# Optimization experiments

Hardware: AMD Instinct MI355X
Metric: run time of the kernel (lower is better)

Reference implementation:

```python
import jax, jax.numpy as jnp
import numpy as np

N_NODES = 100000   # num_nodes
N_EDGES = 50000    # num_hyperedges
M = 1600000        # num incidences
D = 64             # hidden_size
N_LAYERS = 1


def setup_inputs() -> dict:
    key = jax.random.key(0)
    k1, k2, k3 = jax.random.split(key, 3)
    x = jax.random.normal(k1, (N_NODES, D), dtype=jnp.float32)
    node_idx = jax.random.randint(k2, (M,), 0, N_NODES, dtype=jnp.int32)
    edge_idx = jax.random.randint(k3, (M,), 0, N_EDGES, dtype=jnp.int32)
    edge_weight = jnp.ones((N_EDGES,), dtype=jnp.float32)
    return {"x": x, "node_idx": node_idx, "edge_idx": edge_idx, "edge_weight": edge_weight}


def _safe_recip(v):
    # 1/v with inf -> 0, matching D[D==inf]=0
    return jnp.where(v > 0, 1.0 / jnp.where(v > 0, v, 1.0), 0.0)


def _hconv(x, node_idx, edge_idx, edge_weight):
    # D[n] = sum over incidences (n,e) of w[e]; B[e] = hyperedge cardinality
    Dn = jax.ops.segment_sum(edge_weight[edge_idx], node_idx, num_segments=N_NODES)
    Dn = _safe_recip(Dn)
    Be = jax.ops.segment_sum(jnp.ones((node_idx.shape[0],), x.dtype), edge_idx, num_segments=N_EDGES)
    Be = _safe_recip(Be)
    # stage 1: nodes -> hyperedges, message = B[e] * x[j]
    edge_feat = jax.ops.segment_sum(x[node_idx] * Be[edge_idx][:, None], edge_idx, num_segments=N_EDGES)
    # stage 2: hyperedges -> nodes, message = D[i] * edge_feat[e]
    out = jax.ops.segment_sum(edge_feat[edge_idx] * Dn[node_idx][:, None], node_idx, num_segments=N_NODES)
    return out


def reference(x, node_idx, edge_idx, edge_weight):
    h = x
    acc = x
    for _ in range(N_LAYERS):
        h = _hconv(h, node_idx, edge_idx, edge_weight)
        acc = acc + h
    return acc / (N_LAYERS + 1)
```

## Files before the change

kernel.cpp:

```cpp
#include <hip/hip_runtime.h>

#define N_NODES 100000
#define N_EDGES 50000
#define N_KEYS  150000
#define M_INC   1600000
#define D_HID   64

#define SUBR    32
#define SUBLEN  50000
#define KPART   16384
#define PN      7
#define PE      4

#define N_TILES_N 25
#define N_TILES_E 13

typedef float v2f __attribute__((ext_vector_type(2)));


__device__ __forceinline__ unsigned enc_fp8x4(float a, float b, float c, float d) {
    unsigned r = 0;
    r = __builtin_amdgcn_cvt_pk_fp8_f32(a, b, r, false);
    r = __builtin_amdgcn_cvt_pk_fp8_f32(c, d, r, true);
    return r;
}

__global__ __launch_bounds__(1024) void count_kernel(
        const int* __restrict__ node_idx, const int* __restrict__ edge_idx,
        unsigned short* __restrict__ rank_n, unsigned short* __restrict__ rank_e,
        unsigned short* __restrict__ cnt_g) {
    __shared__ unsigned int h[KPART];
    int bid = blockIdx.x;
    const int* idx; unsigned short* rk; int p, s, klim, goff;
    if (bid < PN * SUBR) {
        p = bid / SUBR; s = bid % SUBR;
        idx = node_idx; rk = rank_n; klim = N_NODES; goff = 0;
    } else {
        int b2 = bid - PN * SUBR;
        p = b2 / SUBR; s = b2 % SUBR;
        idx = edge_idx; rk = rank_e; klim = N_EDGES; goff = N_NODES;
    }
    int kbase = p * KPART;
    int t = threadIdx.x;
    for (int i = t; i < KPART; i += 1024) h[i] = 0;
    __syncthreads();
    int mbase = s * SUBLEN;
    const int4* src4 = (const int4*)(idx + mbase);
    for (int i = t; i < SUBLEN / 4; i += 1024) {
        int4 v = src4[i];
        int m0 = mbase + i * 4;
        int k;
        k = v.x - kbase; if ((unsigned)k < KPART) rk[m0 + 0] = (unsigned short)atomicAdd(&h[k], 1u);
        k = v.y - kbase; if ((unsigned)k < KPART) rk[m0 + 1] = (unsigned short)atomicAdd(&h[k], 1u);
        k = v.z - kbase; if ((unsigned)k < KPART) rk[m0 + 2] = (unsigned short)atomicAdd(&h[k], 1u);
        k = v.w - kbase; if ((unsigned)k < KPART) rk[m0 + 3] = (unsigned short)atomicAdd(&h[k], 1u);
    }
    __syncthreads();
    for (int i = t; i < KPART; i += 1024) {
        int key = kbase + i;
        if (key < klim) cnt_g[s * N_KEYS + goff + key] = (unsigned short)h[i];
    }
}

__global__ void replprefix_kernel(const unsigned short* __restrict__ cnt_g,
                                  unsigned short* __restrict__ rb, int* __restrict__ tot) {
    int key = blockIdx.x * 256 + threadIdx.x;
    if (key < N_KEYS) {
        int base = 0;
#pragma unroll
        for (int k = 0; k < SUBR; k++) {
            rb[k * N_KEYS + key] = (unsigned short)base;
            base += (int)cnt_g[k * N_KEYS + key];
        }
        tot[key] = base;
    }
}

__global__ void scan_partial_kernel(const int* __restrict__ cnt,
                                    int* __restrict__ pn, int* __restrict__ pe) {
    __shared__ int lds[16];
    int b = blockIdx.x;
    const int* src; int nElem; int tile; int* dst;
    if (b < N_TILES_N) { src = cnt;            nElem = N_NODES; tile = b;             dst = pn; }
    else               { src = cnt + N_NODES;  nElem = N_EDGES; tile = b - N_TILES_N; dst = pe; }
    int t = threadIdx.x;
    int i4 = tile * 1024 + t;
    int sum = 0;
    if (i4 * 4 < nElem) {
        int4 v = ((const int4*)src)[i4];
        sum = v.x + v.y + v.z + v.w;
    }
    for (int off = 1; off < 64; off <<= 1) sum += __shfl_xor(sum, off, 64);
    if ((t & 63) == 0) lds[t >> 6] = sum;
    __syncthreads();
    if (t < 16) {
        int s = lds[t];
        for (int off = 1; off < 16; off <<= 1) s += __shfl_xor(s, off, 64);
        if (t == 0) dst[tile] = s;
    }
}

__global__ void scan_base_kernel(const int* __restrict__ pn, const int* __restrict__ pe,
                                 int* __restrict__ bn, int* __restrict__ be,
                                 int* __restrict__ noff, int* __restrict__ eoff) {
    int w = threadIdx.x >> 6;
    int lane = threadIdx.x & 63;
    if (w == 0) {
        int v = (lane < N_TILES_N) ? pn[lane] : 0;
        int incl = v;
        for (int d = 1; d < 64; d <<= 1) { int u = __shfl_up(incl, d, 64); if (lane >= d) incl += u; }
        if (lane < N_TILES_N) bn[lane] = incl - v;
        if (lane == N_TILES_N - 1) noff[N_NODES] = incl;
    } else {
        int v = (lane < N_TILES_E) ? pe[lane] : 0;
        int incl = v;
        for (int d = 1; d < 64; d <<= 1) { int u = __shfl_up(incl, d, 64); if (lane >= d) incl += u; }
        if (lane < N_TILES_E) be[lane] = incl - v;
        if (lane == N_TILES_E - 1) eoff[N_EDGES] = incl;
    }
}

__global__ void scan_write_kernel(const int* __restrict__ cnt,
                                  const int* __restrict__ bn, const int* __restrict__ be,
                                  int* __restrict__ noff, int* __restrict__ eoff) {
    __shared__ int wsum[16];
    int b = blockIdx.x;
    const int* src; int* dst; int nElem; int tile; int tbase;
    if (b < N_TILES_N) { src = cnt;           dst = noff; nElem = N_NODES; tile = b;             tbase = bn[tile]; }
    else               { src = cnt + N_NODES; dst = eoff; nElem = N_EDGES; tile = b - N_TILES_N; tbase = be[tile]; }
    int t = threadIdx.x;
    int lane = t & 63, w = t >> 6;
    int i4 = tile * 1024 + t;
    int4 c = make_int4(0, 0, 0, 0);
    bool valid = (i4 * 4 < nElem);
    if (valid) c = ((const int4*)src)[i4];
    int tsum = c.x + c.y + c.z + c.w;
    int incl = tsum;
    for (int d = 1; d < 64; d <<= 1) { int u = __shfl_up(incl, d, 64); if (lane >= d) incl += u; }
    if (lane == 63) wsum[w] = incl;
    __syncthreads();
    if (t < 16) {
        int v = wsum[t];
        int wi = v;
        for (int d = 1; d < 16; d <<= 1) { int u = __shfl_up(wi, d, 64); if (t >= d) wi += u; }
        wsum[t] = wi - v;
    }
    __syncthreads();
    int ex = tbase + wsum[w] + incl - tsum;
    if (valid) {
        int4 o;
        o.x = ex; o.y = ex + c.x; o.z = o.y + c.y; o.w = o.z + c.z;
        ((int4*)dst)[i4] = o;
    }
}

__global__ void fill_kernel(const int* __restrict__ node_idx,
                            const int* __restrict__ edge_idx,
                            const unsigned short* __restrict__ rank_n,
                            const unsigned short* __restrict__ rank_e,
                            const unsigned short* __restrict__ rb,
                            const int* __restrict__ noff, const int* __restrict__ eoff,
                            int* __restrict__ node_csr, int* __restrict__ edge_csr) {
    int q = blockIdx.x * 256 + threadIdx.x;
    if (q < M_INC / 4) {
        int m0 = q * 4;
        int s = m0 / SUBLEN;
        const unsigned short* rbs = rb + s * N_KEYS;
        int4 nv = ((const int4*)node_idx)[q];
        int4 ev = ((const int4*)edge_idx)[q];
        ushort4 rn = ((const ushort4*)rank_n)[q];
        ushort4 re = ((const ushort4*)rank_e)[q];
        node_csr[noff[nv.x] + (int)rbs[nv.x] + (int)rn.x] = ev.x;
        node_csr[noff[nv.y] + (int)rbs[nv.y] + (int)rn.y] = ev.y;
        node_csr[noff[nv.z] + (int)rbs[nv.z] + (int)rn.z] = ev.z;
        node_csr[noff[nv.w] + (int)rbs[nv.w] + (int)rn.w] = ev.w;
        edge_csr[eoff[ev.x] + (int)rbs[N_NODES + ev.x] + (int)re.x] = nv.x;
        edge_csr[eoff[ev.y] + (int)rbs[N_NODES + ev.y] + (int)re.y] = nv.y;
        edge_csr[eoff[ev.z] + (int)rbs[N_NODES + ev.z] + (int)re.z] = nv.z;
        edge_csr[eoff[ev.w] + (int)rbs[N_NODES + ev.w] + (int)re.w] = nv.w;
    }
}

__global__ void cvt_kernel(const float* __restrict__ x, uint2* __restrict__ xh) {
    int i = blockIdx.x * 256 + threadIdx.x;
    if (i < (N_NODES * D_HID) / 8) {
        const float4* x4 = (const float4*)x;
        float4 a = x4[i * 2], b = x4[i * 2 + 1];
        uint2 o;
        o.x = enc_fp8x4(a.x, a.y, a.z, a.w);
        o.y = enc_fp8x4(b.x, b.y, b.z, b.w);
        xh[i] = o;
    }
}

__global__ void stage1_kernel(const int* __restrict__ eoff, const int* __restrict__ ecsr,
                              const uint2* __restrict__ xh, uint2* __restrict__ ef) {
    int wid = (blockIdx.x * 256 + threadIdx.x) >> 6;
    if (wid >= N_EDGES) return;
    int lane = threadIdx.x & 63;
    int group = lane >> 3;
    int gl = lane & 7;
    int s = eoff[wid], t = eoff[wid + 1];
    float acc[8] = {0.f, 0.f, 0.f, 0.f, 0.f, 0.f, 0.f, 0.f};
    for (int base = s; base < t; base += 64) {
        int idx_l = (base + lane < t) ? ecsr[base + lane] : 0;
        int cnt = t - base; if (cnt > 64) cnt = 64;
        int steps = (cnt + 7) >> 3;
        for (int j = 0; j < steps; j++) {
            int p = 8 * j + group;
            int mi = __shfl(idx_l, p, 64);
            if (p < cnt) {
                uint2 v = xh[(size_t)mi * 8 + gl];
                v2f d0 = __builtin_amdgcn_cvt_pk_f32_fp8(v.x, false);
                v2f d1 = __builtin_amdgcn_cvt_pk_f32_fp8(v.x, true);
                v2f d2 = __builtin_amdgcn_cvt_pk_f32_fp8(v.y, false);
                v2f d3 = __builtin_amdgcn_cvt_pk_f32_fp8(v.y, true);
                acc[0] += d0.x; acc[1] += d0.y; acc[2] += d1.x; acc[3] += d1.y;
                acc[4] += d2.x; acc[5] += d2.y; acc[6] += d3.x; acc[7] += d3.y;
            }
        }
    }
    for (int off = 8; off < 64; off <<= 1)
#pragma unroll
        for (int i = 0; i < 8; i++) acc[i] += __shfl_xor(acc[i], off, 64);
    if (group == 0) {
        int card = t - s;
        float ber = (card > 0) ? (1.0f / (float)card) : 0.f;
        uint2 o;
        o.x = enc_fp8x4(acc[0] * ber, acc[1] * ber, acc[2] * ber, acc[3] * ber);
        o.y = enc_fp8x4(acc[4] * ber, acc[5] * ber, acc[6] * ber, acc[7] * ber);
        ef[(size_t)wid * 8 + gl] = o;
    }
}

__global__ void stage2_kernel(const int* __restrict__ noff, const int* __restrict__ ncsr,
                              const uint2* __restrict__ ef, const float* __restrict__ ew,
                              const float* __restrict__ x, float* __restrict__ out) {
    int wid = (blockIdx.x * 256 + threadIdx.x) >> 6;
    if (wid >= N_NODES) return;
    int lane = threadIdx.x & 63;
    int group = lane >> 3;
    int gl = lane & 7;
    int s = noff[wid], t = noff[wid + 1];
    float acc[8] = {0.f, 0.f, 0.f, 0.f, 0.f, 0.f, 0.f, 0.f};
    float dn = 0.f;
    for (int base = s; base < t; base += 64) {
        bool lv = (base + lane < t);
        int idx_l = lv ? ncsr[base + lane] : 0;
        if (lv) dn += ew[idx_l];
        int cnt = t - base; if (cnt > 64) cnt = 64;
        int steps = (cnt + 7) >> 3;
        for (int j = 0; j < steps; j++) {
            int p = 8 * j + group;
            int mi = __shfl(idx_l, p, 64);
            if (p < cnt) {
                uint2 v = ef[(size_t)mi * 8 + gl];
                v2f d0 = __builtin_amdgcn_cvt_pk_f32_fp8(v.x, false);
                v2f d1 = __builtin_amdgcn_cvt_pk_f32_fp8(v.x, true);
                v2f d2 = __builtin_amdgcn_cvt_pk_f32_fp8(v.y, false);
                v2f d3 = __builtin_amdgcn_cvt_pk_f32_fp8(v.y, true);
                acc[0] += d0.x; acc[1] += d0.y; acc[2] += d1.x; acc[3] += d1.y;
                acc[4] += d2.x; acc[5] += d2.y; acc[6] += d3.x; acc[7] += d3.y;
            }
        }
    }
    for (int off = 1; off < 64; off <<= 1) dn += __shfl_xor(dn, off, 64);
    for (int off = 8; off < 64; off <<= 1)
#pragma unroll
        for (int i = 0; i < 8; i++) acc[i] += __shfl_xor(acc[i], off, 64);
    if (group == 0) {
        float dnr = (dn > 0.f) ? (1.0f / dn) : 0.f;
        const float4* x4 = (const float4*)x;
        float4* o4 = (float4*)out;
        float4 a = x4[(size_t)wid * 16 + gl * 2];
        float4 b = x4[(size_t)wid * 16 + gl * 2 + 1];
        float4 ra, rb2;
        ra.x = 0.5f * (a.x + dnr * acc[0]);
        ra.y = 0.5f * (a.y + dnr * acc[1]);
        ra.z = 0.5f * (a.z + dnr * acc[2]);
        ra.w = 0.5f * (a.w + dnr * acc[3]);
        rb2.x = 0.5f * (b.x + dnr * acc[4]);
        rb2.y = 0.5f * (b.y + dnr * acc[5]);
        rb2.z = 0.5f * (b.z + dnr * acc[6]);
        rb2.w = 0.5f * (b.w + dnr * acc[7]);
        o4[(size_t)wid * 16 + gl * 2] = ra;
        o4[(size_t)wid * 16 + gl * 2 + 1] = rb2;
    }
}

extern "C" void kernel_launch(void* const* d_in, const int* in_sizes, int n_in,
                              void* d_out, int out_size, void* d_ws, size_t ws_size,
                              hipStream_t stream) {
    const float* x        = (const float*)d_in[0];
    const int*   node_idx = (const int*)d_in[1];
    const int*   edge_idx = (const int*)d_in[2];
    const float* ew       = (const float*)d_in[3];
    float* out = (float*)d_out;

    char* ws = (char*)d_ws;
    unsigned short* rank_n   = (unsigned short*)(ws + 0);
    unsigned short* rank_e   = (unsigned short*)(ws + 3200000);
    int*            noff     = (int*)(ws + 6400000);
    int*            eoff     = (int*)(ws + 6800016);
    int*            node_csr = (int*)(ws + 7000032);
    int*            edge_csr = (int*)(ws + 13400032);
    unsigned short* cnt_g = (unsigned short*)(ws + 7000032);
    unsigned short* rb    = (unsigned short*)(ws + 19800032);
    int*            pn    = (int*)(ws + 29400032);
    int*            pe    = pn + 32;
    int*            bn    = pn + 64;
    int*            be    = pn + 96;
    int*            tot   = (int*)(ws + 29404128);
    uint2*          ef    = (uint2*)(ws + 0);
    uint2*          xh    = (uint2*)(ws + 19800032);

    count_kernel<<<(PN + PE) * SUBR, 1024, 0, stream>>>(node_idx, edge_idx, rank_n, rank_e, cnt_g);
    replprefix_kernel<<<(N_KEYS + 255) / 256, 256, 0, stream>>>(cnt_g, rb, tot);
    scan_partial_kernel<<<N_TILES_N + N_TILES_E, 1024, 0, stream>>>(tot, pn, pe);
    scan_base_kernel<<<1, 128, 0, stream>>>(pn, pe, bn, be, noff, eoff);
    scan_write_kernel<<<N_TILES_N + N_TILES_E, 1024, 0, stream>>>(tot, bn, be, noff, eoff);
    fill_kernel<<<(M_INC / 4 + 255) / 256, 256, 0, stream>>>(node_idx, edge_idx, rank_n, rank_e,
                                                             rb, noff, eoff, node_csr, edge_csr);
    cvt_kernel<<<((N_NODES * D_HID / 8) + 255) / 256, 256, 0, stream>>>(x, xh);
    stage1_kernel<<<(N_EDGES * 64 + 255) / 256, 256, 0, stream>>>(eoff, edge_csr, xh, ef);
    stage2_kernel<<<(N_NODES * 64 + 255) / 256, 256, 0, stream>>>(noff, node_csr, ef, ew, x, out);
}
```

Before: 258.1 us.

## Replace deterministic ranked CSR build with global atomic histogram and atomic fill

Swaps the LDS-partitioned count kernel, per-subrange rank arrays and replicated prefix kernel for a single global-atomic histogram. The fill then claims slots with atomicAdd on per-key cursors, and each block group handles one eighth of the key range to spread the atomics. This removes the replprefix pass and the rank and rb traffic. In exchange it adds many global atomics, makes the order within each CSR row nondeterministic (so float sums may vary run to run), and has every block reread the index arrays.

```diff
diff --git a/kernel.cpp b/kernel.cpp
--- a/kernel.cpp
+++ b/kernel.cpp
@@ -6,14 +6,12 @@
 #define M_INC   1600000
 #define D_HID   64
 
-#define SUBR    32
-#define SUBLEN  50000
-#define KPART   16384
-#define PN      7
-#define PE      4
-
 #define N_TILES_N 25
 #define N_TILES_E 13
+
+#define FILL_BLOCKS 1024
+#define NSLICE (N_NODES / 8)
+#define ESLICE (N_EDGES / 8)
 
 typedef float v2f __attribute__((ext_vector_type(2)));
 
@@ -25,54 +23,21 @@
     return r;
 }
 
-__global__ __launch_bounds__(1024) void count_kernel(
-        const int* __restrict__ node_idx, const int* __restrict__ edge_idx,
-        unsigned short* __restrict__ rank_n, unsigned short* __restrict__ rank_e,
-        unsigned short* __restrict__ cnt_g) {
-    __shared__ unsigned int h[KPART];
-    int bid = blockIdx.x;
-    const int* idx; unsigned short* rk; int p, s, klim, goff;
-    if (bid < PN * SUBR) {
-        p = bid / SUBR; s = bid % SUBR;
-        idx = node_idx; rk = rank_n; klim = N_NODES; goff = 0;
-    } else {
-        int b2 = bid - PN * SUBR;
-        p = b2 / SUBR; s = b2 % SUBR;
-        idx = edge_idx; rk = rank_e; klim = N_EDGES; goff = N_NODES;
-    }
-    int kbase = p * KPART;
-    int t = threadIdx.x;
-    for (int i = t; i < KPART; i += 1024) h[i] = 0;
-    __syncthreads();
-    int mbase = s * SUBLEN;
-    const int4* src4 = (const int4*)(idx + mbase);
-    for (int i = t; i < SUBLEN / 4; i += 1024) {
-        int4 v = src4[i];
-        int m0 = mbase + i * 4;
-        int k;
-        k = v.x - kbase; if ((unsigned)k < KPART) rk[m0 + 0] = (unsigned short)atomicAdd(&h[k], 1u);
-        k = v.y - kbase; if ((unsigned)k < KPART) rk[m0 + 1] = (unsigned short)atomicAdd(&h[k], 1u);
-        k = v.z - kbase; if ((unsigned)k < KPART) rk[m0 + 2] = (unsigned short)atomicAdd(&h[k], 1u);
-        k = v.w - kbase; if ((unsigned)k < KPART) rk[m0 + 3] = (unsigned short)atomicAdd(&h[k], 1u);
-    }
-    __syncthreads();
-    for (int i = t; i < KPART; i += 1024) {
-        int key = kbase + i;
-        if (key < klim) cnt_g[s * N_KEYS + goff + key] = (unsigned short)h[i];
-    }
-}
-
-__global__ void replprefix_kernel(const unsigned short* __restrict__ cnt_g,
-                                  unsigned short* __restrict__ rb, int* __restrict__ tot) {
-    int key = blockIdx.x * 256 + threadIdx.x;
-    if (key < N_KEYS) {
-        int base = 0;
-#pragma unroll
-        for (int k = 0; k < SUBR; k++) {
-            rb[k * N_KEYS + key] = (unsigned short)base;
-            base += (int)cnt_g[k * N_KEYS + key];
-        }
-        tot[key] = base;
+__global__ __launch_bounds__(256) void hist_kernel(const int* __restrict__ node_idx,
+                                                   const int* __restrict__ edge_idx,
+                                                   int* __restrict__ cnt) {
+    int i = blockIdx.x * 256 + threadIdx.x;
+    if (i < M_INC / 4) {
+        int4 nv = ((const int4*)node_idx)[i];
+        int4 ev = ((const int4*)edge_idx)[i];
+        atomicAdd(&cnt[nv.x], 1);
+        atomicAdd(&cnt[nv.y], 1);
+        atomicAdd(&cnt[nv.z], 1);
+        atomicAdd(&cnt[nv.w], 1);
+        atomicAdd(&cnt[N_NODES + ev.x], 1);
+        atomicAdd(&cnt[N_NODES + ev.y], 1);
+        atomicAdd(&cnt[N_NODES + ev.z], 1);
+        atomicAdd(&cnt[N_NODES + ev.w], 1);
     }
 }
 
@@ -122,12 +87,13 @@
 
 __global__ void scan_write_kernel(const int* __restrict__ cnt,
                                   const int* __restrict__ bn, const int* __restrict__ be,
-                                  int* __restrict__ noff, int* __restrict__ eoff) {
+                                  int* __restrict__ noff, int* __restrict__ eoff,
+                                  int* __restrict__ pos) {
     __shared__ int wsum[16];
     int b = blockIdx.x;
-    const int* src; int* dst; int nElem; int tile; int tbase;
-    if (b < N_TILES_N) { src = cnt;           dst = noff; nElem = N_NODES; tile = b;             tbase = bn[tile]; }
-    else               { src = cnt + N_NODES; dst = eoff; nElem = N_EDGES; tile = b - N_TILES_N; tbase = be[tile]; }
+    const int* src; int* dst; int* pdst; int nElem; int tile; int tbase;
+    if (b < N_TILES_N) { src = cnt;           dst = noff; pdst = pos;           nElem = N_NODES; tile = b;             tbase = bn[tile]; }
+    else               { src = cnt + N_NODES; dst = eoff; pdst = pos + N_NODES; nElem = N_EDGES; tile = b - N_TILES_N; tbase = be[tile]; }
     int t = threadIdx.x;
     int lane = t & 63, w = t >> 6;
     int i4 = tile * 1024 + t;
@@ -151,33 +117,38 @@
         int4 o;
         o.x = ex; o.y = ex + c.x; o.z = o.y + c.y; o.w = o.z + c.z;
         ((int4*)dst)[i4] = o;
-    }
-}
-
-__global__ void fill_kernel(const int* __restrict__ node_idx,
-                            const int* __restrict__ edge_idx,
-                            const unsigned short* __restrict__ rank_n,
-                            const unsigned short* __restrict__ rank_e,
-                            const unsigned short* __restrict__ rb,
-                            const int* __restrict__ noff, const int* __restrict__ eoff,
-                            int* __restrict__ node_csr, int* __restrict__ edge_csr) {
-    int q = blockIdx.x * 256 + threadIdx.x;
-    if (q < M_INC / 4) {
-        int m0 = q * 4;
-        int s = m0 / SUBLEN;
-        const unsigned short* rbs = rb + s * N_KEYS;
-        int4 nv = ((const int4*)node_idx)[q];
-        int4 ev = ((const int4*)edge_idx)[q];
-        ushort4 rn = ((const ushort4*)rank_n)[q];
-        ushort4 re = ((const ushort4*)rank_e)[q];
-        node_csr[noff[nv.x] + (int)rbs[nv.x] + (int)rn.x] = ev.x;
-        node_csr[noff[nv.y] + (int)rbs[nv.y] + (int)rn.y] = ev.y;
-        node_csr[noff[nv.z] + (int)rbs[nv.z] + (int)rn.z] = ev.z;
-        node_csr[noff[nv.w] + (int)rbs[nv.w] + (int)rn.w] = ev.w;
-        edge_csr[eoff[ev.x] + (int)rbs[N_NODES + ev.x] + (int)re.x] = nv.x;
-        edge_csr[eoff[ev.y] + (int)rbs[N_NODES + ev.y] + (int)re.y] = nv.y;
-        edge_csr[eoff[ev.z] + (int)rbs[N_NODES + ev.z] + (int)re.z] = nv.z;
-        edge_csr[eoff[ev.w] + (int)rbs[N_NODES + ev.w] + (int)re.w] = nv.w;
+        ((int4*)pdst)[i4] = o;
+    }
+}
+
+__global__ __launch_bounds__(256) void fill_kernel(
+        const int* __restrict__ node_idx, const int* __restrict__ edge_idx,
+        int* __restrict__ pos, int* __restrict__ node_csr, int* __restrict__ edge_csr) {
+    const int g = blockIdx.x & 7;
+    const int w = blockIdx.x >> 3;
+    int t = w * 256 + (int)threadIdx.x;
+    const int nlo = g * NSLICE;
+    const int elo = g * ESLICE;
+    const int4* n4 = (const int4*)node_idx;
+    const int4* e4 = (const int4*)edge_idx;
+    int* __restrict__ pose = pos + N_NODES;
+    const int stride = (FILL_BLOCKS / 8) * 256;
+    for (int i = t; i < M_INC / 4; i += stride) {
+        int4 nv = n4[i];
+        int4 ev = e4[i];
+        int n, e;
+        n = nv.x; e = ev.x;
+        if ((unsigned)(n - nlo) < (unsigned)NSLICE) node_csr[atomicAdd(&pos[n], 1)] = e;
+        if ((unsigned)(e - elo) < (unsigned)ESLICE) edge_csr[atomicAdd(&pose[e], 1)] = n;
+        n = nv.y; e = ev.y;
+        if ((unsigned)(n - nlo) < (unsigned)NSLICE) node_csr[atomicAdd(&pos[n], 1)] = e;
+        if ((unsigned)(e - elo) < (unsigned)ESLICE) edge_csr[atomicAdd(&pose[e], 1)] = n;
+        n = nv.z; e = ev.z;
+        if ((unsigned)(n - nlo) < (unsigned)NSLICE) node_csr[atomicAdd(&pos[n], 1)] = e;
+        if ((unsigned)(e - elo) < (unsigned)ESLICE) edge_csr[atomicAdd(&pose[e], 1)] = n;
+        n = nv.w; e = ev.w;
+        if ((unsigned)(n - nlo) < (unsigned)NSLICE) node_csr[atomicAdd(&pos[n], 1)] = e;
+        if ((unsigned)(e - elo) < (unsigned)ESLICE) edge_csr[atomicAdd(&pose[e], 1)] = n;
     }
 }
 
@@ -298,29 +269,25 @@
     float* out = (float*)d_out;
 
     char* ws = (char*)d_ws;
-    unsigned short* rank_n   = (unsigned short*)(ws + 0);
-    unsigned short* rank_e   = (unsigned short*)(ws + 3200000);
-    int*            noff     = (int*)(ws + 6400000);
-    int*            eoff     = (int*)(ws + 6800016);
-    int*            node_csr = (int*)(ws + 7000032);
-    int*            edge_csr = (int*)(ws + 13400032);
-    unsigned short* cnt_g = (unsigned short*)(ws + 7000032);
-    unsigned short* rb    = (unsigned short*)(ws + 19800032);
-    int*            pn    = (int*)(ws + 29400032);
-    int*            pe    = pn + 32;
-    int*            bn    = pn + 64;
-    int*            be    = pn + 96;
-    int*            tot   = (int*)(ws + 29404128);
-    uint2*          ef    = (uint2*)(ws + 0);
-    uint2*          xh    = (uint2*)(ws + 19800032);
-
-    count_kernel<<<(PN + PE) * SUBR, 1024, 0, stream>>>(node_idx, edge_idx, rank_n, rank_e, cnt_g);
-    replprefix_kernel<<<(N_KEYS + 255) / 256, 256, 0, stream>>>(cnt_g, rb, tot);
-    scan_partial_kernel<<<N_TILES_N + N_TILES_E, 1024, 0, stream>>>(tot, pn, pe);
+    int*            cnt      = (int*)(ws + 0);
+    int*            pos      = (int*)(ws + 600000);
+    int*            noff     = (int*)(ws + 1200000);
+    int*            eoff     = (int*)(ws + 1600016);
+    int*            pn       = (int*)(ws + 1800032);
+    int*            pe       = pn + 32;
+    int*            bn       = pn + 64;
+    int*            be       = pn + 96;
+    int*            node_csr = (int*)(ws + 1900032);
+    int*            edge_csr = (int*)(ws + 8300032);
+    uint2*          xh       = (uint2*)(ws + 14700032);
+    uint2*          ef       = (uint2*)(ws + 21100032);
+
+    hipMemsetAsync(cnt, 0, N_KEYS * sizeof(int), stream);
+    hist_kernel<<<(M_INC / 4 + 255) / 256, 256, 0, stream>>>(node_idx, edge_idx, cnt);
+    scan_partial_kernel<<<N_TILES_N + N_TILES_E, 1024, 0, stream>>>(cnt, pn, pe);
     scan_base_kernel<<<1, 128, 0, stream>>>(pn, pe, bn, be, noff, eoff);
-    scan_write_kernel<<<N_TILES_N + N_TILES_E, 1024, 0, stream>>>(tot, bn, be, noff, eoff);
-    fill_kernel<<<(M_INC / 4 + 255) / 256, 256, 0, stream>>>(node_idx, edge_idx, rank_n, rank_e,
-                                                             rb, noff, eoff, node_csr, edge_csr);
+    scan_write_kernel<<<N_TILES_N + N_TILES_E, 1024, 0, stream>>>(cnt, bn, be, noff, eoff, pos);
+    fill_kernel<<<FILL_BLOCKS, 256, 0, stream>>>(node_idx, edge_idx, pos, node_csr, edge_csr);
     cvt_kernel<<<((N_NODES * D_HID / 8) + 255) / 256, 256, 0, stream>>>(x, xh);
     stage1_kernel<<<(N_EDGES * 64 + 255) / 256, 256, 0, stream>>>(eoff, edge_csr, xh, ef);
     stage2_kernel<<<(N_NODES * 64 + 255) / 256, 256, 0, stream>>>(noff, node_csr, ef, ew, x, out);
```

Result: slower. 436.8 us (+69.3%).

## Partition CSR fill scatter into eight key-range groups for write locality

Applied to the files above, without the earlier changes.

The fill kernel becomes grid-stride with 1024 blocks split into eight groups. Each group rereads all incidences but scatters only entries whose node or edge id falls in its slice, so each group's scattered writes hit a narrower address range. This should improve cache or XCD-local write locality. Input loads use nontemporal hints. In exchange the index and rank arrays are read eight times and each thread runs more comparisons.

```diff
diff --git a/kernel.cpp b/kernel.cpp
--- a/kernel.cpp
+++ b/kernel.cpp
@@ -15,7 +15,13 @@
 #define N_TILES_N 25
 #define N_TILES_E 13
 
+#define FILL_BLOCKS 1024
+#define NSLICE (N_NODES / 8)
+#define ESLICE (N_EDGES / 8)
+
 typedef float v2f __attribute__((ext_vector_type(2)));
+typedef int i4v __attribute__((ext_vector_type(4)));
+typedef unsigned short u16x4 __attribute__((ext_vector_type(4)));
 
 
 __device__ __forceinline__ unsigned enc_fp8x4(float a, float b, float c, float d) {
@@ -154,30 +160,42 @@
     }
 }
 
-__global__ void fill_kernel(const int* __restrict__ node_idx,
-                            const int* __restrict__ edge_idx,
-                            const unsigned short* __restrict__ rank_n,
-                            const unsigned short* __restrict__ rank_e,
-                            const unsigned short* __restrict__ rb,
-                            const int* __restrict__ noff, const int* __restrict__ eoff,
-                            int* __restrict__ node_csr, int* __restrict__ edge_csr) {
-    int q = blockIdx.x * 256 + threadIdx.x;
-    if (q < M_INC / 4) {
-        int m0 = q * 4;
-        int s = m0 / SUBLEN;
+__global__ __launch_bounds__(256) void fill_kernel(
+        const int* __restrict__ node_idx, const int* __restrict__ edge_idx,
+        const unsigned short* __restrict__ rank_n, const unsigned short* __restrict__ rank_e,
+        const unsigned short* __restrict__ rb,
+        const int* __restrict__ noff, const int* __restrict__ eoff,
+        int* __restrict__ node_csr, int* __restrict__ edge_csr) {
+    const int g = blockIdx.x & 7;
+    const int w = blockIdx.x >> 3;
+    int t0 = w * 256 + (int)threadIdx.x;
+    const int nlo = g * NSLICE;
+    const int elo = g * ESLICE;
+    const i4v* n4 = (const i4v*)node_idx;
+    const i4v* e4 = (const i4v*)edge_idx;
+    const u16x4* rn4 = (const u16x4*)rank_n;
+    const u16x4* re4 = (const u16x4*)rank_e;
+    const int stride = (FILL_BLOCKS / 8) * 256;
+    for (int q = t0; q < M_INC / 4; q += stride) {
+        int s = (q * 4) / SUBLEN;
         const unsigned short* rbs = rb + s * N_KEYS;
-        int4 nv = ((const int4*)node_idx)[q];
-        int4 ev = ((const int4*)edge_idx)[q];
-        ushort4 rn = ((const ushort4*)rank_n)[q];
-        ushort4 re = ((const ushort4*)rank_e)[q];
-        node_csr[noff[nv.x] + (int)rbs[nv.x] + (int)rn.x] = ev.x;
-        node_csr[noff[nv.y] + (int)rbs[nv.y] + (int)rn.y] = ev.y;
-        node_csr[noff[nv.z] + (int)rbs[nv.z] + (int)rn.z] = ev.z;
-        node_csr[noff[nv.w] + (int)rbs[nv.w] + (int)rn.w] = ev.w;
-        edge_csr[eoff[ev.x] + (int)rbs[N_NODES + ev.x] + (int)re.x] = nv.x;
-        edge_csr[eoff[ev.y] + (int)rbs[N_NODES + ev.y] + (int)re.y] = nv.y;
-        edge_csr[eoff[ev.z] + (int)rbs[N_NODES + ev.z] + (int)re.z] = nv.z;
-        edge_csr[eoff[ev.w] + (int)rbs[N_NODES + ev.w] + (int)re.w] = nv.w;
+        i4v nv = __builtin_nontemporal_load(&n4[q]);
+        i4v ev = __builtin_nontemporal_load(&e4[q]);
+        u16x4 rn = __builtin_nontemporal_load(&rn4[q]);
+        u16x4 re = __builtin_nontemporal_load(&re4[q]);
+        int n, e;
+        n = nv.x; e = ev.x;
+        if ((unsigned)(n - nlo) < (unsigned)NSLICE) node_csr[noff[n] + (int)rbs[n] + (int)rn.x] = e;
+        if ((unsigned)(e - elo) < (unsigned)ESLICE) edge_csr[eoff[e] + (int)rbs[N_NODES + e] + (int)re.x] = n;
+        n = nv.y; e = ev.y;
+        if ((unsigned)(n - nlo) < (unsigned)NSLICE) node_csr[noff[n] + (int)rbs[n] + (int)rn.y] = e;
+        if ((unsigned)(e - elo) < (unsigned)ESLICE) edge_csr[eoff[e] + (int)rbs[N_NODES + e] + (int)re.y] = n;
+        n = nv.z; e = ev.z;
+        if ((unsigned)(n - nlo) < (unsigned)NSLICE) node_csr[noff[n] + (int)rbs[n] + (int)rn.z] = e;
+        if ((unsigned)(e - elo) < (unsigned)ESLICE) edge_csr[eoff[e] + (int)rbs[N_NODES + e] + (int)re.z] = n;
+        n = nv.w; e = ev.w;
+        if ((unsigned)(n - nlo) < (unsigned)NSLICE) node_csr[noff[n] + (int)rbs[n] + (int)rn.w] = e;
+        if ((unsigned)(e - elo) < (unsigned)ESLICE) edge_csr[eoff[e] + (int)rbs[N_NODES + e] + (int)re.w] = n;
     }
 }
 
@@ -319,8 +337,8 @@
     scan_partial_kernel<<<N_TILES_N + N_TILES_E, 1024, 0, stream>>>(tot, pn, pe);
     scan_base_kernel<<<1, 128, 0, stream>>>(pn, pe, bn, be, noff, eoff);
     scan_write_kernel<<<N_TILES_N + N_TILES_E, 1024, 0, stream>>>(tot, bn, be, noff, eoff);
-    fill_kernel<<<(M_INC / 4 + 255) / 256, 256, 0, stream>>>(node_idx, edge_idx, rank_n, rank_e,
-                                                             rb, noff, eoff, node_csr, edge_csr);
+    fill_kernel<<<FILL_BLOCKS, 256, 0, stream>>>(node_idx, edge_idx, rank_n, rank_e,
+                                                 rb, noff, eoff, node_csr, edge_csr);
     cvt_kernel<<<((N_NODES * D_HID / 8) + 255) / 256, 256, 0, stream>>>(x, xh);
     stage1_kernel<<<(N_EDGES * 64 + 255) / 256, 256, 0, stream>>>(eoff, edge_csr, xh, ef);
     stage2_kernel<<<(N_NODES * 64 + 255) / 256, 256, 0, stream>>>(noff, node_csr, ef, ew, x, out);
```

Result: slower. 267.9 us (+3.8%).
